# Optimization experiments

Measured on AMD Instinct MI355X. Metric: run time of the kernel, lower is better.

Reference implementation:

```python
import jax, jax.numpy as jnp
import numpy as np


def _sobel_filters():
    # 3D Sobel kernels for x, y, z directions, shape (3, 1, 3, 3, 3) in OIDHW.
    x = np.array([[[-1, 0, 1], [-2, 0, 2], [-1, 0, 1]],
                  [[-2, 0, 2], [-4, 0, 4], [-2, 0, 2]],
                  [[-1, 0, 1], [-2, 0, 2], [-1, 0, 1]]], dtype=np.float32)
    y = np.array([[[1, 2, 1], [0, 0, 0], [-1, -2, -1]],
                  [[2, 4, 2], [0, 0, 0], [-2, -4, -2]],
                  [[1, 2, 1], [0, 0, 0], [-1, -2, -1]]], dtype=np.float32)
    z = np.array([[[1, 2, 1], [2, 4, 2], [1, 2, 1]],
                  [[0, 0, 0], [0, 0, 0], [0, 0, 0]],
                  [[-1, -2, -1], [-2, -4, -2], [-1, -2, -1]]], dtype=np.float32)
    return jnp.asarray(np.stack([x, y, z])[:, None])  # (3,1,3,3,3)


_FILTERS = _sobel_filters()
_EPS = 1e-10


def gradient3d(x):
    # x: [B,1,D,H,W] -> gradient magnitude [B,1,D,H,W].
    # Single conv with 3 output channels == three separate torch conv3d + concat.
    g = jax.lax.conv_general_dilated(
        x, _FILTERS, window_strides=(1, 1, 1),
        padding=[(1, 1), (1, 1), (1, 1)],
        dimension_numbers=('NCDHW', 'OIDHW', 'NCDHW'))  # [B,3,D,H,W]
    return jnp.sqrt(jnp.sum(g * g, axis=1, keepdims=True) + _EPS)


def setup_inputs() -> dict:
    key = jax.random.key(0)
    k1, k2, k3 = jax.random.split(key, 3)
    shape = (2, 1, 192, 192, 192)
    pred = jax.random.normal(k1, shape, dtype=jnp.float32)
    gt_dose = jax.random.normal(k2, shape, dtype=jnp.float32)
    body_mask = (jax.random.uniform(k3, shape) > 0.3).astype(jnp.float32)
    return {"pred": pred, "gt_dose": gt_dose, "body_mask": body_mask}


def reference(pred, gt_dose, body_mask):
    mse = jnp.square(pred - gt_dose) * body_mask
    mge = jnp.square(gradient3d(gt_dose) - gradient3d(pred)) * body_mask
    return jnp.mean(mse + jnp.tanh(mge) * mse)
```

## Files before the change

### kernel.cpp

```cpp
#include <hip/hip_runtime.h>
#include <math.h>

#define W 192
#define H 192
#define DEPTH 192
#define BATCH 2
#define DC 12
#define HW (H * W)
#define VOL ((size_t)DEPTH * HW)
#define ROWT 48
#define ROWSB 4
#define BLOCKT (ROWT * ROWSB)
#define ROUNDS (DC + 2)


__global__ __launch_bounds__(BLOCKT, 3) void sobel_loss_part(
    const float* __restrict__ pred, const float* __restrict__ gt,
    const float* __restrict__ mask, float* __restrict__ partials)
{
    const int tid = threadIdx.x;
    const int rt = tid / ROWT;
    const int ct = tid - rt * ROWT;
    const int wc = 4 * ct;
    const int h  = blockIdx.x * ROWSB + rt;
    const int d0 = blockIdx.y * DC;
    const size_t base = (size_t)blockIdx.z * VOL;

    const bool lok = (wc > 0);
    const bool rok = (wc + 4 < W);
    const bool y0ok = (h > 0);
    const bool y2ok = (h + 1 < H);
    const int g1 = h * W + wc;
    const int g0 = g1 - W, g2 = g1 + W;

    float AX[2][4], BX[2][4], AY[2][4], BY[2][4], AZ[2][4], BZ[2][4];
    #pragma unroll
    for (int a = 0; a < 2; ++a)
        #pragma unroll
        for (int c = 0; c < 4; ++c) {
            AX[a][c]=BX[a][c]=AY[a][c]=BY[a][c]=AZ[a][c]=BZ[a][c]=0.f;
        }

    float Pc[4] = {0,0,0,0}, Gc[4] = {0,0,0,0};
    float acc = 0.f;

    #pragma unroll 2
    for (int t = 0; t < ROUNDS; ++t) {
        const int p = d0 - 1 + t;
        const bool pv = (p >= 0) && (p < DEPTH);
        const size_t pb = base + (size_t)(pv ? p : 0) * HW;

        float outx[2][4], outy[2][4], outz[2][4];
        float mid[2][4];

        #pragma unroll
        for (int a = 0; a < 2; ++a) {
            const float* __restrict__ src = a ? gt : pred;
            const bool r0 = pv && y0ok, r1 = pv, r2 = pv && y2ok;
            float4 m0 = r0 ? *(const float4*)(src + pb + g0) : make_float4(0,0,0,0);
            float4 m1 = r1 ? *(const float4*)(src + pb + g1) : make_float4(0,0,0,0);
            float4 m2 = r2 ? *(const float4*)(src + pb + g2) : make_float4(0,0,0,0);
            float v[3][6];
            v[0][0] = (r0 && lok) ? src[pb + g0 - 1] : 0.f;
            v[0][5] = (r0 && rok) ? src[pb + g0 + 4] : 0.f;
            v[1][0] = (r1 && lok) ? src[pb + g1 - 1] : 0.f;
            v[1][5] = (r1 && rok) ? src[pb + g1 + 4] : 0.f;
            v[2][0] = (r2 && lok) ? src[pb + g2 - 1] : 0.f;
            v[2][5] = (r2 && rok) ? src[pb + g2 + 4] : 0.f;
            v[0][1]=m0.x; v[0][2]=m0.y; v[0][3]=m0.z; v[0][4]=m0.w;
            v[1][1]=m1.x; v[1][2]=m1.y; v[1][3]=m1.z; v[1][4]=m1.w;
            v[2][1]=m2.x; v[2][2]=m2.y; v[2][3]=m2.z; v[2][4]=m2.w;
            mid[a][0]=m1.x; mid[a][1]=m1.y; mid[a][2]=m1.z; mid[a][3]=m1.w;

            float sh[3][4], dh[3][4];
            #pragma unroll
            for (int r = 0; r < 3; ++r)
                #pragma unroll
                for (int c = 0; c < 4; ++c) {
                    sh[r][c] = v[r][c] + 2.f * v[r][c+1] + v[r][c+2];
                    dh[r][c] = v[r][c+2] - v[r][c];
                }
            #pragma unroll
            for (int c = 0; c < 4; ++c) {
                float qdx = dh[0][c] + 2.f * dh[1][c] + dh[2][c];
                float qsx = sh[0][c] + 2.f * sh[1][c] + sh[2][c];
                float qdy = sh[0][c] - sh[2][c];
                outx[a][c] = AX[a][c] + qdx;
                AX[a][c]   = fmaf(2.f, qdx, BX[a][c]);
                BX[a][c]   = qdx;
                outy[a][c] = AY[a][c] + qdy;
                AY[a][c]   = fmaf(2.f, qdy, BY[a][c]);
                BY[a][c]   = qdy;
                outz[a][c] = AZ[a][c] - qsx;
                AZ[a][c]   = BZ[a][c];
                BZ[a][c]   = qsx;
            }
        }

        if (t >= 2) {
            const int od = p - 1;
            const float4 M4 = *(const float4*)(mask + base + (size_t)od * HW + g1);
            const float mv[4] = {M4.x, M4.y, M4.z, M4.w};
            #pragma unroll
            for (int c = 0; c < 4; ++c) {
                float ga = __builtin_amdgcn_sqrtf(
                    fmaf(outz[0][c], outz[0][c],
                    fmaf(outy[0][c], outy[0][c],
                    fmaf(outx[0][c], outx[0][c], 1e-10f))));
                float gb = __builtin_amdgcn_sqrtf(
                    fmaf(outz[1][c], outz[1][c],
                    fmaf(outy[1][c], outy[1][c],
                    fmaf(outx[1][c], outx[1][c], 1e-10f))));
                float m   = mv[c];
                float dm  = Pc[c] - Gc[c];
                float mse = dm * dm * m;
                float dg  = gb - ga;
                float mge = dg * dg * m;
                float ex = __expf(mge + mge);
                float rc = __builtin_amdgcn_rcpf(ex + 1.f);
                acc = fmaf(mse, fmaf(-2.f, rc, 2.f), acc);
            }
        }
        #pragma unroll
        for (int c = 0; c < 4; ++c) { Pc[c] = mid[0][c]; Gc[c] = mid[1][c]; }
    }

    float v = acc;
    #pragma unroll
    for (int o = 32; o > 0; o >>= 1) v += __shfl_down(v, o, 64);
    __shared__ float red[3];
    if ((tid & 63) == 0) red[tid >> 6] = v;
    __syncthreads();
    if (tid == 0) {
        partials[(size_t)blockIdx.z * (gridDim.x * gridDim.y)
                 + (size_t)blockIdx.y * gridDim.x + blockIdx.x]
            = red[0] + red[1] + red[2];
    }
}

__global__ __launch_bounds__(256) void reduce_final(
    const float* __restrict__ partials, int n, float* __restrict__ out)
{
    int tid = threadIdx.x;
    double s = 0.0;
    for (int i = tid; i < n; i += 256) s += (double)partials[i];
    #pragma unroll
    for (int o = 32; o > 0; o >>= 1) s += __shfl_down(s, o, 64);
    __shared__ double red[4];
    if ((tid & 63) == 0) red[tid >> 6] = s;
    __syncthreads();
    if (tid == 0) {
        double t = red[0] + red[1] + red[2] + red[3];
        const double ntot = (double)BATCH * (double)DEPTH * (double)H * (double)W;
        out[0] = (float)(t / ntot);
    }
}

extern "C" void kernel_launch(void* const* d_in, const int* in_sizes, int n_in,
                              void* d_out, int out_size, void* d_ws, size_t ws_size,
                              hipStream_t stream) {
    const float* pred = (const float*)d_in[0];
    const float* gt   = (const float*)d_in[1];
    const float* mask = (const float*)d_in[2];
    float* partials = (float*)d_ws;

    dim3 grid(H / ROWSB, DEPTH / DC, BATCH);
    sobel_loss_part<<<grid, BLOCKT, 0, stream>>>(pred, gt, mask, partials);

    int nparts = grid.x * grid.y * grid.z;
    reduce_final<<<1, 256, 0, stream>>>(partials, nparts, (float*)d_out);
}
```

Baseline: 215.7 us.

## Double-buffer plane loads in registers and halve depth chunk per block

Adds register double-buffering so each depth plane's pred/gt stencil loads and mask loads are issued one iteration ahead of their use, overlapping global memory latency with the Sobel arithmetic. It also halves the depth chunk per block, doubling the grid size for more parallelism. The prefetch buffers raise register pressure, which under launch_bounds(...,3) may cause spills. The smaller chunk raises the halo re-read overhead from 14/12 to 8/6 planes per block.

```diff
diff --git a/kernel.cpp b/kernel.cpp
--- a/kernel.cpp
+++ b/kernel.cpp
@@ -5,7 +5,7 @@
 #define H 192
 #define DEPTH 192
 #define BATCH 2
-#define DC 12
+#define DC 6
 #define HW (H * W)
 #define VOL ((size_t)DEPTH * HW)
 #define ROWT 48
@@ -26,12 +26,33 @@
     const int d0 = blockIdx.y * DC;
     const size_t base = (size_t)blockIdx.z * VOL;
 
-    const bool lok = (wc > 0);
-    const bool rok = (wc + 4 < W);
-    const bool y0ok = (h > 0);
-    const bool y2ok = (h + 1 < H);
+    const bool lok = (wc > 0), rok = (wc + 4 < W);
+    const bool y0ok = (h > 0), y2ok = (h + 1 < H);
     const int g1 = h * W + wc;
     const int g0 = g1 - W, g2 = g1 + W;
+
+    float4 Rm0[2][2], Rm1[2][2], Rm2[2][2];
+    float  Rl0[2][2], Rl1[2][2], Rl2[2][2];
+    float  Rr0[2][2], Rr1[2][2], Rr2[2][2];
+
+    auto load_plane = [&](int p, int buf) {
+        const bool pv = (p >= 0) && (p < DEPTH);
+        const size_t pb = base + (size_t)(pv ? p : 0) * HW;
+        #pragma unroll
+        for (int a = 0; a < 2; ++a) {
+            const float* __restrict__ s = a ? gt : pred;
+            const bool b0 = pv && y0ok, b1 = pv, b2 = pv && y2ok;
+            Rm0[buf][a] = b0 ? *(const float4*)(s + pb + g0) : make_float4(0,0,0,0);
+            Rm1[buf][a] = b1 ? *(const float4*)(s + pb + g1) : make_float4(0,0,0,0);
+            Rm2[buf][a] = b2 ? *(const float4*)(s + pb + g2) : make_float4(0,0,0,0);
+            Rl0[buf][a] = (b0 && lok) ? s[pb + g0 - 1] : 0.f;
+            Rl1[buf][a] = (b1 && lok) ? s[pb + g1 - 1] : 0.f;
+            Rl2[buf][a] = (b2 && lok) ? s[pb + g2 - 1] : 0.f;
+            Rr0[buf][a] = (b0 && rok) ? s[pb + g0 + 4] : 0.f;
+            Rr1[buf][a] = (b1 && rok) ? s[pb + g1 + 4] : 0.f;
+            Rr2[buf][a] = (b2 && rok) ? s[pb + g2 + 4] : 0.f;
+        }
+    };
 
     float AX[2][4], BX[2][4], AY[2][4], BY[2][4], AZ[2][4], BZ[2][4];
     #pragma unroll
@@ -42,31 +63,32 @@
         }
 
     float Pc[4] = {0,0,0,0}, Gc[4] = {0,0,0,0};
+    float4 Mn = make_float4(0,0,0,0), Mc;
     float acc = 0.f;
+
+    load_plane(d0 - 1, 0);
 
     #pragma unroll 2
     for (int t = 0; t < ROUNDS; ++t) {
+        const int buf = t & 1;
+
+        if (t + 1 < ROUNDS) load_plane(d0 + t, buf ^ 1);
+
+        Mc = Mn;
+        if (t >= 1 && t <= DC)
+            Mn = *(const float4*)(mask + base + (size_t)(d0 + t - 1) * HW + g1);
+
         const int p = d0 - 1 + t;
-        const bool pv = (p >= 0) && (p < DEPTH);
-        const size_t pb = base + (size_t)(pv ? p : 0) * HW;
-
         float outx[2][4], outy[2][4], outz[2][4];
         float mid[2][4];
 
         #pragma unroll
         for (int a = 0; a < 2; ++a) {
-            const float* __restrict__ src = a ? gt : pred;
-            const bool r0 = pv && y0ok, r1 = pv, r2 = pv && y2ok;
-            float4 m0 = r0 ? *(const float4*)(src + pb + g0) : make_float4(0,0,0,0);
-            float4 m1 = r1 ? *(const float4*)(src + pb + g1) : make_float4(0,0,0,0);
-            float4 m2 = r2 ? *(const float4*)(src + pb + g2) : make_float4(0,0,0,0);
+            float4 m0 = Rm0[buf][a], m1 = Rm1[buf][a], m2 = Rm2[buf][a];
             float v[3][6];
-            v[0][0] = (r0 && lok) ? src[pb + g0 - 1] : 0.f;
-            v[0][5] = (r0 && rok) ? src[pb + g0 + 4] : 0.f;
-            v[1][0] = (r1 && lok) ? src[pb + g1 - 1] : 0.f;
-            v[1][5] = (r1 && rok) ? src[pb + g1 + 4] : 0.f;
-            v[2][0] = (r2 && lok) ? src[pb + g2 - 1] : 0.f;
-            v[2][5] = (r2 && rok) ? src[pb + g2 + 4] : 0.f;
+            v[0][0]=Rl0[buf][a]; v[0][5]=Rr0[buf][a];
+            v[1][0]=Rl1[buf][a]; v[1][5]=Rr1[buf][a];
+            v[2][0]=Rl2[buf][a]; v[2][5]=Rr2[buf][a];
             v[0][1]=m0.x; v[0][2]=m0.y; v[0][3]=m0.z; v[0][4]=m0.w;
             v[1][1]=m1.x; v[1][2]=m1.y; v[1][3]=m1.z; v[1][4]=m1.w;
             v[2][1]=m2.x; v[2][2]=m2.y; v[2][3]=m2.z; v[2][4]=m2.w;
@@ -98,9 +120,7 @@
         }
 
         if (t >= 2) {
-            const int od = p - 1;
-            const float4 M4 = *(const float4*)(mask + base + (size_t)od * HW + g1);
-            const float mv[4] = {M4.x, M4.y, M4.z, M4.w};
+            const float mv[4] = {Mc.x, Mc.y, Mc.z, Mc.w};
             #pragma unroll
             for (int c = 0; c < 4; ++c) {
                 float ga = __builtin_amdgcn_sqrtf(
@@ -121,6 +141,7 @@
                 acc = fmaf(mse, fmaf(-2.f, rc, 2.f), acc);
             }
         }
+
         #pragma unroll
         for (int c = 0; c < 4; ++c) { Pc[c] = mid[0][c]; Gc[c] = mid[1][c]; }
     }
```

Result: slower. 340.7 us (+57.9%).
